# Kernel tuning notes

Measured on AMD Instinct MI355X. Metric: run time of the kernel, lower is better.

## Reference

```python
import jax, jax.numpy as jnp
import numpy as np

EPSILON = 1e-8
NUM_STEPS = 1000
S_OFFSET = 0.0001
POWER = 2
CLIPMAX = 0.999
B = 1048576


def _schedule():
    t = jnp.arange(0, NUM_STEPS + 1, dtype=jnp.float32)
    f_t = jnp.cos(np.pi / 2 * (t / NUM_STEPS + S_OFFSET) / (1 + S_OFFSET)) ** POWER
    alpha_bars = f_t / f_t[0]
    betas = jnp.concatenate([jnp.zeros([1], jnp.float32), 1.0 - alpha_bars[1:] / alpha_bars[:-1]])
    betas = jnp.minimum(betas, CLIPMAX)
    sigmas = jnp.sqrt(betas[1:] * ((1.0 - alpha_bars[:-1]) / (1.0 - alpha_bars[1:])))
    sigmas = jnp.concatenate([jnp.zeros([1], jnp.float32), sigmas])
    return alpha_bars, betas, sigmas


def setup_inputs() -> dict:
    key = jax.random.key(0)
    k1, k2, k3, k4, k5 = jax.random.split(key, 5)
    lt = jax.random.normal(k1, (B, 6), dtype=jnp.float32)
    predicted_l0 = jax.random.normal(k2, (B, 6), dtype=jnp.float32)
    pred_lattice = jax.random.normal(k3, (B, 3, 3), dtype=jnp.float32)
    z_noise = jax.random.normal(k4, (B, 6), dtype=jnp.float32)  # torch.randn_like(lt), frozen
    t = jax.random.randint(k5, (B,), 0, NUM_STEPS, dtype=jnp.int64)
    alpha_bars, betas, sigmas = _schedule()
    return {
        "lt": lt,
        "predicted_l0": predicted_l0,
        "pred_lattice": pred_lattice,
        "alpha_bars": alpha_bars,
        "betas": betas,
        "sigmas": sigmas,
        "z_noise": z_noise,
        "t": t,
    }


def reference(lt, predicted_l0, pred_lattice, alpha_bars, betas, sigmas, z_noise, t):
    # VP_lattice.reverse
    alpha = 1.0 - betas[t]
    alpha = jnp.maximum(alpha, 1.0 - betas[-2])  # clamp_min
    alpha_bar = alpha_bars[t]
    sigma = sigmas[t][:, None]

    # polar_decomposition: only the symmetric factor L_tilda = V diag(S) V^T is used
    _, S, Vt = jnp.linalg.svd(pred_lattice, full_matrices=False)  # (B,3),(B,3,3)
    L = jnp.einsum("bji,bj,bjk->bik", Vt, S, Vt)  # Vt^T @ diag(S) @ Vt
    L = (L + jnp.swapaxes(L, 1, 2)) / 2  # symmetrize

    # symmetric_matrix_to_vector: upper triangular incl. diagonal
    vec = jnp.stack([L[:, 0, 0], L[:, 0, 1], L[:, 0, 2], L[:, 1, 1], L[:, 1, 2], L[:, 2, 2]], axis=1)

    predicted_noise = lt - (vec + predicted_l0) / 2
    z = jnp.where((t > 1)[:, None], z_noise, jnp.zeros_like(z_noise))
    coef = (1.0 / jnp.sqrt(alpha + EPSILON))[:, None]
    scale = ((1.0 - alpha) / jnp.sqrt(1.0 - alpha_bar + EPSILON))[:, None]
    return coef * (lt - scale * predicted_noise) + sigma * z
```

## Files before the change

### kernel.cpp

```cpp
#include <hip/hip_runtime.h>


#define NUM_STEPS 1000
#define TBL 1008
#define BLOCK 256

__global__ __launch_bounds__(256) void sched_kernel(
    const float* __restrict__ alpha_bars,
    const float* __restrict__ betas,
    const float* __restrict__ sigmas,
    float* __restrict__ ws)
{
    int j = blockIdx.x * blockDim.x + threadIdx.x;
    if (j >= TBL) return;
    if (j <= NUM_STEPS) {
        float beta_last = betas[NUM_STEPS - 1];
        float alpha = 1.0f - fminf(betas[j], beta_last);
        float coef  = 1.0f / sqrtf(alpha + 1e-8f);
        float scale = (1.0f - alpha) / sqrtf(1.0f - alpha_bars[j] + 1e-8f);
        ws[j]           = coef * (1.0f - scale);
        ws[TBL + j]     = 0.5f * coef * scale;
        ws[2 * TBL + j] = (j > 1) ? sigmas[j] : 0.0f;
    } else {
        ws[j] = 0.0f; ws[TBL + j] = 0.0f; ws[2 * TBL + j] = 0.0f;
    }
}

__global__ __launch_bounds__(BLOCK, 6) void vp_lattice_kernel(
    const float* __restrict__ lt,
    const float* __restrict__ pl0,
    const float* __restrict__ plat,
    const float* __restrict__ alpha_bars,
    const float* __restrict__ betas,
    const float* __restrict__ sigmas,
    const float* __restrict__ z_noise,
    const int*   __restrict__ t,
    float* __restrict__ out,
    int n,
    const float* __restrict__ ws,
    int use_ws)
{
    __shared__ __align__(16) float sA[TBL];
    __shared__ __align__(16) float sB[TBL];
    __shared__ __align__(16) float sS[TBL];
    __shared__ __align__(16) float platT[BLOCK * 9];

    const int tid = threadIdx.x;
    const int rowBase = blockIdx.x * BLOCK;
    int rem = n - rowBase; if (rem > BLOCK) rem = BLOCK;

    if (rem == BLOCK) {
        const float4* g9 = reinterpret_cast<const float4*>(plat + (size_t)rowBase * 9);
        float4*       s9 = reinterpret_cast<float4*>(platT);
#pragma unroll
        for (int k = 0; k < 3; ++k) {
            int j = tid + k * BLOCK;
            if (j < BLOCK * 9 / 4) s9[j] = g9[j];
        }
    } else {
        for (int j = tid; j < rem * 9; j += BLOCK)
            platT[j] = plat[(size_t)rowBase * 9 + j];
    }

    if (use_ws) {
        const float4* w4 = reinterpret_cast<const float4*>(ws);
        float4* a4 = reinterpret_cast<float4*>(sA);
        float4* b4 = reinterpret_cast<float4*>(sB);
        float4* s4 = reinterpret_cast<float4*>(sS);
        for (int j = tid; j < TBL / 4; j += BLOCK) {
            a4[j] = w4[j];
            b4[j] = w4[TBL / 4 + j];
            s4[j] = w4[2 * (TBL / 4) + j];
        }
    } else {
        float beta_last = betas[NUM_STEPS - 1];
        for (int j = tid; j < TBL; j += BLOCK) {
            float A = 0.0f, Bc = 0.0f, S = 0.0f;
            if (j <= NUM_STEPS) {
                float alpha = 1.0f - fminf(betas[j], beta_last);
                float coef  = 1.0f / sqrtf(alpha + 1e-8f);
                float scale = (1.0f - alpha) / sqrtf(1.0f - alpha_bars[j] + 1e-8f);
                A  = coef * (1.0f - scale);
                Bc = 0.5f * coef * scale;
                S  = (j > 1) ? sigmas[j] : 0.0f;
            }
            sA[j] = A; sB[j] = Bc; sS[j] = S;
        }
    }

    int ti = (tid < rem) ? t[rowBase + tid] : 0;

    __syncthreads();

    if (tid >= rem) return;

    size_t b6 = (size_t)(rowBase + tid) * 6;
    const float2* lt2 = reinterpret_cast<const float2*>(lt + b6);
    const float2* p02 = reinterpret_cast<const float2*>(pl0 + b6);
    const float2* zn2 = reinterpret_cast<const float2*>(z_noise + b6);
    float2 lw0 = lt2[0], lw1 = lt2[1], lw2 = lt2[2];
    float2 pw0 = p02[0], pw1 = p02[1], pw2 = p02[2];
    float2 zw0 = zn2[0], zw1 = zn2[1], zw2 = zn2[2];

    const float* pr = platT + tid * 9;
    float a00 = pr[0], a01 = pr[1], a02 = pr[2];
    float a10 = pr[3], a11 = pr[4], a12 = pr[5];
    float a20 = pr[6], a21 = pr[7], a22 = pr[8];

    float m00 = a00*a00 + a10*a10 + a20*a20;
    float m01 = a00*a01 + a10*a11 + a20*a21;
    float m02 = a00*a02 + a10*a12 + a20*a22;
    float m11 = a01*a01 + a11*a11 + a21*a21;
    float m12 = a01*a02 + a11*a12 + a21*a22;
    float m22 = a02*a02 + a12*a12 + a22*a22;

    float q  = (m00 + m11 + m22) * (1.0f/3.0f);
    float b00 = m00 - q, b11 = m11 - q, b22 = m22 - q;
    float p1 = m01*m01 + m02*m02 + m12*m12;
    float p2 = b00*b00 + b11*b11 + b22*b22 + 2.0f*p1;
    float p  = sqrtf(p2 * (1.0f/6.0f));
    float detB = b00*(b11*b22 - m12*m12)
               - m01*(m01*b22 - m12*m02)
               + m02*(m01*m12 - b11*m02);
    float pinv = __fdividef(1.0f, fmaxf(p, 1e-20f));
    float r = 0.5f * detB * pinv * pinv * pinv;
    r = fminf(fmaxf(r, -1.0f), 1.0f);

    float ar = fabsf(r);
    float sq = sqrtf(1.0f - ar);
    float pl = 1.5707288f + ar * (-0.2121144f + ar * (0.0742610f - ar * 0.0187293f));
    float ac = sq * pl;
    float acr = (r >= 0.0f) ? ac : (3.14159265358979f - ac);
    float phi = acr * (1.0f/3.0f);
    float mu1 = q + 2.0f*p*__cosf(phi);
    float mu3 = q + 2.0f*p*__cosf(phi + 2.0943951023931953f);
    float mu2 = 3.0f*q - mu1 - mu3;
    float l1 = sqrtf(fmaxf(mu1, 0.0f));
    float l2 = sqrtf(fmaxf(mu2, 0.0f));
    float l3 = sqrtf(fmaxf(mu3, 0.0f));

    float IU   = l1 + l2 + l3;
    float IIU  = l1*(l2 + l3) + l2*l3;
    float IIIU = l1*l2*l3;
    float denom = (l1 + l2) * (l1 + l3) * (l2 + l3);
    float dinv  = __fdividef(1.0f, fmaxf(denom, 1e-25f));
    float sd = (IU*IU - IIU) * dinv;
    float td = IU * IIIU * dinv;
    float nd = -dinv;

    float mm00 = m00*m00 + m01*m01 + m02*m02;
    float mm01 = m00*m01 + m01*m11 + m02*m12;
    float mm02 = m00*m02 + m01*m12 + m02*m22;
    float mm11 = m01*m01 + m11*m11 + m12*m12;
    float mm12 = m01*m02 + m11*m12 + m12*m22;
    float mm22 = m02*m02 + m12*m12 + m22*m22;

    float v0 = nd*mm00 + sd*m00 + td;
    float v1 = nd*mm01 + sd*m01;
    float v2 = nd*mm02 + sd*m02;
    float v3 = nd*mm11 + sd*m11 + td;
    float v4 = nd*mm12 + sd*m12;
    float v5 = nd*mm22 + sd*m22 + td;

    float A  = sA[ti];
    float Bc = sB[ti];
    float S  = sS[ti];

    float2 o0, o1, o2;
    o0.x = A*lw0.x + Bc*(v0 + pw0.x) + S*zw0.x;
    o0.y = A*lw0.y + Bc*(v1 + pw0.y) + S*zw0.y;
    o1.x = A*lw1.x + Bc*(v2 + pw1.x) + S*zw1.x;
    o1.y = A*lw1.y + Bc*(v3 + pw1.y) + S*zw1.y;
    o2.x = A*lw2.x + Bc*(v4 + pw2.x) + S*zw2.x;
    o2.y = A*lw2.y + Bc*(v5 + pw2.y) + S*zw2.y;

    float2* out2 = reinterpret_cast<float2*>(out + b6);
    out2[0] = o0;
    out2[1] = o1;
    out2[2] = o2;
}

extern "C" void kernel_launch(void* const* d_in, const int* in_sizes, int n_in,
                              void* d_out, int out_size, void* d_ws, size_t ws_size,
                              hipStream_t stream) {
    const float* lt         = (const float*)d_in[0];
    const float* pl0        = (const float*)d_in[1];
    const float* plat       = (const float*)d_in[2];
    const float* alpha_bars = (const float*)d_in[3];
    const float* betas      = (const float*)d_in[4];
    const float* sigmas     = (const float*)d_in[5];
    const float* z_noise    = (const float*)d_in[6];
    const int*   t          = (const int*)d_in[7];
    float* out = (float*)d_out;
    float* ws  = (float*)d_ws;

    int n = in_sizes[0] / 6;
    int use_ws = (ws != nullptr && ws_size >= (size_t)(3 * TBL * sizeof(float)));

    if (use_ws) {
        sched_kernel<<<(TBL + 255) / 256, 256, 0, stream>>>(alpha_bars, betas, sigmas, ws);
    }
    int grid = (n + BLOCK - 1) / BLOCK;
    vp_lattice_kernel<<<grid, BLOCK, 0, stream>>>(
        lt, pl0, plat, alpha_bars, betas, sigmas, z_noise, t, out, n, ws, use_ws);
}
```

Before: 154.8 us.

## Process two rows per thread with float4 vectorized loads and stores

Result: no change. 155.0 us (+0.2%).

```diff
diff --git a/kernel.cpp b/kernel.cpp
--- a/kernel.cpp
+++ b/kernel.cpp
@@ -4,6 +4,8 @@
 #define NUM_STEPS 1000
 #define TBL 1008
 #define BLOCK 256
+#define ROWS 2
+#define RPB (BLOCK * ROWS)
 
 __global__ __launch_bounds__(256) void sched_kernel(
     const float* __restrict__ alpha_bars,
@@ -26,7 +28,70 @@
     }
 }
 
-__global__ __launch_bounds__(BLOCK, 6) void vp_lattice_kernel(
+__device__ __forceinline__ void sqrtm_vec(const float* __restrict__ pr,
+                                          float vv[6])
+{
+    float a00 = pr[0], a01 = pr[1], a02 = pr[2];
+    float a10 = pr[3], a11 = pr[4], a12 = pr[5];
+    float a20 = pr[6], a21 = pr[7], a22 = pr[8];
+
+    float m00 = a00*a00 + a10*a10 + a20*a20;
+    float m01 = a00*a01 + a10*a11 + a20*a21;
+    float m02 = a00*a02 + a10*a12 + a20*a22;
+    float m11 = a01*a01 + a11*a11 + a21*a21;
+    float m12 = a01*a02 + a11*a12 + a21*a22;
+    float m22 = a02*a02 + a12*a12 + a22*a22;
+
+    float q  = (m00 + m11 + m22) * (1.0f/3.0f);
+    float b00 = m00 - q, b11 = m11 - q, b22 = m22 - q;
+    float p1 = m01*m01 + m02*m02 + m12*m12;
+    float p2 = b00*b00 + b11*b11 + b22*b22 + 2.0f*p1;
+    float p  = sqrtf(p2 * (1.0f/6.0f));
+    float detB = b00*(b11*b22 - m12*m12)
+               - m01*(m01*b22 - m12*m02)
+               + m02*(m01*m12 - b11*m02);
+    float pinv = __fdividef(1.0f, fmaxf(p, 1e-20f));
+    float r = 0.5f * detB * pinv * pinv * pinv;
+    r = fminf(fmaxf(r, -1.0f), 1.0f);
+
+    float ar = fabsf(r);
+    float sq = sqrtf(1.0f - ar);
+    float pl = 1.5707288f + ar * (-0.2121144f + ar * (0.0742610f - ar * 0.0187293f));
+    float ac = sq * pl;
+    float acr = (r >= 0.0f) ? ac : (3.14159265358979f - ac);
+    float phi = acr * (1.0f/3.0f);
+    float mu1 = q + 2.0f*p*__cosf(phi);
+    float mu3 = q + 2.0f*p*__cosf(phi + 2.0943951023931953f);
+    float mu2 = 3.0f*q - mu1 - mu3;
+    float l1 = sqrtf(fmaxf(mu1, 0.0f));
+    float l2 = sqrtf(fmaxf(mu2, 0.0f));
+    float l3 = sqrtf(fmaxf(mu3, 0.0f));
+
+    float IU   = l1 + l2 + l3;
+    float IIU  = l1*(l2 + l3) + l2*l3;
+    float IIIU = l1*l2*l3;
+    float denom = (l1 + l2) * (l1 + l3) * (l2 + l3);
+    float dinv  = __fdividef(1.0f, fmaxf(denom, 1e-25f));
+    float sd = (IU*IU - IIU) * dinv;
+    float td = IU * IIIU * dinv;
+    float nd = -dinv;
+
+    float mm00 = m00*m00 + m01*m01 + m02*m02;
+    float mm01 = m00*m01 + m01*m11 + m02*m12;
+    float mm02 = m00*m02 + m01*m12 + m02*m22;
+    float mm11 = m01*m01 + m11*m11 + m12*m12;
+    float mm12 = m01*m02 + m11*m12 + m12*m22;
+    float mm22 = m02*m02 + m12*m12 + m22*m22;
+
+    vv[0] = nd*mm00 + sd*m00 + td;
+    vv[1] = nd*mm01 + sd*m01;
+    vv[2] = nd*mm02 + sd*m02;
+    vv[3] = nd*mm11 + sd*m11 + td;
+    vv[4] = nd*mm12 + sd*m12;
+    vv[5] = nd*mm22 + sd*m22 + td;
+}
+
+__global__ __launch_bounds__(BLOCK, 5) void vp_lattice_kernel(
     const float* __restrict__ lt,
     const float* __restrict__ pl0,
     const float* __restrict__ plat,
@@ -43,19 +108,20 @@
     __shared__ __align__(16) float sA[TBL];
     __shared__ __align__(16) float sB[TBL];
     __shared__ __align__(16) float sS[TBL];
-    __shared__ __align__(16) float platT[BLOCK * 9];
+    __shared__ __align__(16) float platT[RPB * 9];
 
     const int tid = threadIdx.x;
-    const int rowBase = blockIdx.x * BLOCK;
-    int rem = n - rowBase; if (rem > BLOCK) rem = BLOCK;
-
-    if (rem == BLOCK) {
+    const int rowBase = blockIdx.x * RPB;
+    int rem = n - rowBase; if (rem > RPB) rem = RPB;
+    const bool full = (rem == RPB);
+
+    if (full) {
         const float4* g9 = reinterpret_cast<const float4*>(plat + (size_t)rowBase * 9);
         float4*       s9 = reinterpret_cast<float4*>(platT);
 #pragma unroll
-        for (int k = 0; k < 3; ++k) {
+        for (int k = 0; k < 5; ++k) {
             int j = tid + k * BLOCK;
-            if (j < BLOCK * 9 / 4) s9[j] = g9[j];
+            if (j < RPB * 9 / 4) s9[j] = g9[j];
         }
     } else {
         for (int j = tid; j < rem * 9; j += BLOCK)
@@ -88,96 +154,79 @@
         }
     }
 
-    int ti = (tid < rem) ? t[rowBase + tid] : 0;
+    const int r0 = rowBase + 2 * tid;
+    int ti0 = 0, ti1 = 0;
+    float4 lv0, lv1, lv2, pv0, pv1, pv2, zv0, zv1, zv2;
+    lv0 = lv1 = lv2 = pv0 = pv1 = pv2 = zv0 = zv1 = zv2 = make_float4(0.f,0.f,0.f,0.f);
+
+    if (full) {
+        int2 tp = *(reinterpret_cast<const int2*>(t + rowBase) + tid);
+        ti0 = tp.x; ti1 = tp.y;
+        const float4* lp = reinterpret_cast<const float4*>(lt      + (size_t)rowBase * 6) + tid * 3;
+        const float4* pp = reinterpret_cast<const float4*>(pl0     + (size_t)rowBase * 6) + tid * 3;
+        const float4* zp = reinterpret_cast<const float4*>(z_noise + (size_t)rowBase * 6) + tid * 3;
+        lv0 = lp[0]; lv1 = lp[1]; lv2 = lp[2];
+        pv0 = pp[0]; pv1 = pp[1]; pv2 = pp[2];
+        zv0 = zp[0]; zv1 = zp[1]; zv2 = zp[2];
+    } else {
+        float lbuf[12] = {0}, pbuf[12] = {0}, zbuf[12] = {0};
+        for (int c = 0; c < 12; ++c) {
+            size_t idx = (size_t)r0 * 6 + c;
+            if (r0 * 6 + c < rem * 6 + rowBase * 6 && (r0 + c / 6) < n) {
+                lbuf[c] = lt[idx]; pbuf[c] = pl0[idx]; zbuf[c] = z_noise[idx];
+            }
+        }
+        lv0 = make_float4(lbuf[0], lbuf[1], lbuf[2], lbuf[3]);
+        lv1 = make_float4(lbuf[4], lbuf[5], lbuf[6], lbuf[7]);
+        lv2 = make_float4(lbuf[8], lbuf[9], lbuf[10], lbuf[11]);
+        pv0 = make_float4(pbuf[0], pbuf[1], pbuf[2], pbuf[3]);
+        pv1 = make_float4(pbuf[4], pbuf[5], pbuf[6], pbuf[7]);
+        pv2 = make_float4(pbuf[8], pbuf[9], pbuf[10], pbuf[11]);
+        zv0 = make_float4(zbuf[0], zbuf[1], zbuf[2], zbuf[3]);
+        zv1 = make_float4(zbuf[4], zbuf[5], zbuf[6], zbuf[7]);
+        zv2 = make_float4(zbuf[8], zbuf[9], zbuf[10], zbuf[11]);
+        if (r0     < n) ti0 = t[r0];
+        if (r0 + 1 < n) ti1 = t[r0 + 1];
+    }
 
     __syncthreads();
 
-    if (tid >= rem) return;
-
-    size_t b6 = (size_t)(rowBase + tid) * 6;
-    const float2* lt2 = reinterpret_cast<const float2*>(lt + b6);
-    const float2* p02 = reinterpret_cast<const float2*>(pl0 + b6);
-    const float2* zn2 = reinterpret_cast<const float2*>(z_noise + b6);
-    float2 lw0 = lt2[0], lw1 = lt2[1], lw2 = lt2[2];
-    float2 pw0 = p02[0], pw1 = p02[1], pw2 = p02[2];
-    float2 zw0 = zn2[0], zw1 = zn2[1], zw2 = zn2[2];
-
-    const float* pr = platT + tid * 9;
-    float a00 = pr[0], a01 = pr[1], a02 = pr[2];
-    float a10 = pr[3], a11 = pr[4], a12 = pr[5];
-    float a20 = pr[6], a21 = pr[7], a22 = pr[8];
-
-    float m00 = a00*a00 + a10*a10 + a20*a20;
-    float m01 = a00*a01 + a10*a11 + a20*a21;
-    float m02 = a00*a02 + a10*a12 + a20*a22;
-    float m11 = a01*a01 + a11*a11 + a21*a21;
-    float m12 = a01*a02 + a11*a12 + a21*a22;
-    float m22 = a02*a02 + a12*a12 + a22*a22;
-
-    float q  = (m00 + m11 + m22) * (1.0f/3.0f);
-    float b00 = m00 - q, b11 = m11 - q, b22 = m22 - q;
-    float p1 = m01*m01 + m02*m02 + m12*m12;
-    float p2 = b00*b00 + b11*b11 + b22*b22 + 2.0f*p1;
-    float p  = sqrtf(p2 * (1.0f/6.0f));
-    float detB = b00*(b11*b22 - m12*m12)
-               - m01*(m01*b22 - m12*m02)
-               + m02*(m01*m12 - b11*m02);
-    float pinv = __fdividef(1.0f, fmaxf(p, 1e-20f));
-    float r = 0.5f * detB * pinv * pinv * pinv;
-    r = fminf(fmaxf(r, -1.0f), 1.0f);
-
-    float ar = fabsf(r);
-    float sq = sqrtf(1.0f - ar);
-    float pl = 1.5707288f + ar * (-0.2121144f + ar * (0.0742610f - ar * 0.0187293f));
-    float ac = sq * pl;
-    float acr = (r >= 0.0f) ? ac : (3.14159265358979f - ac);
-    float phi = acr * (1.0f/3.0f);
-    float mu1 = q + 2.0f*p*__cosf(phi);
-    float mu3 = q + 2.0f*p*__cosf(phi + 2.0943951023931953f);
-    float mu2 = 3.0f*q - mu1 - mu3;
-    float l1 = sqrtf(fmaxf(mu1, 0.0f));
-    float l2 = sqrtf(fmaxf(mu2, 0.0f));
-    float l3 = sqrtf(fmaxf(mu3, 0.0f));
-
-    float IU   = l1 + l2 + l3;
-    float IIU  = l1*(l2 + l3) + l2*l3;
-    float IIIU = l1*l2*l3;
-    float denom = (l1 + l2) * (l1 + l3) * (l2 + l3);
-    float dinv  = __fdividef(1.0f, fmaxf(denom, 1e-25f));
-    float sd = (IU*IU - IIU) * dinv;
-    float td = IU * IIIU * dinv;
-    float nd = -dinv;
-
-    float mm00 = m00*m00 + m01*m01 + m02*m02;
-    float mm01 = m00*m01 + m01*m11 + m02*m12;
-    float mm02 = m00*m02 + m01*m12 + m02*m22;
-    float mm11 = m01*m01 + m11*m11 + m12*m12;
-    float mm12 = m01*m02 + m11*m12 + m12*m22;
-    float mm22 = m02*m02 + m12*m12 + m22*m22;
-
-    float v0 = nd*mm00 + sd*m00 + td;
-    float v1 = nd*mm01 + sd*m01;
-    float v2 = nd*mm02 + sd*m02;
-    float v3 = nd*mm11 + sd*m11 + td;
-    float v4 = nd*mm12 + sd*m12;
-    float v5 = nd*mm22 + sd*m22 + td;
-
-    float A  = sA[ti];
-    float Bc = sB[ti];
-    float S  = sS[ti];
-
-    float2 o0, o1, o2;
-    o0.x = A*lw0.x + Bc*(v0 + pw0.x) + S*zw0.x;
-    o0.y = A*lw0.y + Bc*(v1 + pw0.y) + S*zw0.y;
-    o1.x = A*lw1.x + Bc*(v2 + pw1.x) + S*zw1.x;
-    o1.y = A*lw1.y + Bc*(v3 + pw1.y) + S*zw1.y;
-    o2.x = A*lw2.x + Bc*(v4 + pw2.x) + S*zw2.x;
-    o2.y = A*lw2.y + Bc*(v5 + pw2.y) + S*zw2.y;
-
-    float2* out2 = reinterpret_cast<float2*>(out + b6);
-    out2[0] = o0;
-    out2[1] = o1;
-    out2[2] = o2;
+    if (r0 >= n) return;
+
+    float va[6];
+    sqrtm_vec(platT + tid * 18, va);
+    float A0 = sA[ti0], B0 = sB[ti0], S0 = sS[ti0];
+
+    float o[12];
+    o[0] = A0*lv0.x + B0*(va[0] + pv0.x) + S0*zv0.x;
+    o[1] = A0*lv0.y + B0*(va[1] + pv0.y) + S0*zv0.y;
+    o[2] = A0*lv0.z + B0*(va[2] + pv0.z) + S0*zv0.z;
+    o[3] = A0*lv0.w + B0*(va[3] + pv0.w) + S0*zv0.w;
+    o[4] = A0*lv1.x + B0*(va[4] + pv1.x) + S0*zv1.x;
+    o[5] = A0*lv1.y + B0*(va[5] + pv1.y) + S0*zv1.y;
+
+    bool has1 = (r0 + 1 < n);
+    if (has1) {
+        float vb[6];
+        sqrtm_vec(platT + tid * 18 + 9, vb);
+        float A1 = sA[ti1], B1 = sB[ti1], S1 = sS[ti1];
+        o[6]  = A1*lv1.z + B1*(vb[0] + pv1.z) + S1*zv1.z;
+        o[7]  = A1*lv1.w + B1*(vb[1] + pv1.w) + S1*zv1.w;
+        o[8]  = A1*lv2.x + B1*(vb[2] + pv2.x) + S1*zv2.x;
+        o[9]  = A1*lv2.y + B1*(vb[3] + pv2.y) + S1*zv2.y;
+        o[10] = A1*lv2.z + B1*(vb[4] + pv2.z) + S1*zv2.z;
+        o[11] = A1*lv2.w + B1*(vb[5] + pv2.w) + S1*zv2.w;
+    }
+
+    if (full) {
+        float4* op = reinterpret_cast<float4*>(out + (size_t)rowBase * 6) + tid * 3;
+        op[0] = make_float4(o[0], o[1], o[2],  o[3]);
+        op[1] = make_float4(o[4], o[5], o[6],  o[7]);
+        op[2] = make_float4(o[8], o[9], o[10], o[11]);
+    } else {
+        int lim = has1 ? 12 : 6;
+        for (int c = 0; c < lim; ++c) out[(size_t)r0 * 6 + c] = o[c];
+    }
 }
 
 extern "C" void kernel_launch(void* const* d_in, const int* in_sizes, int n_in,
@@ -200,7 +249,7 @@
     if (use_ws) {
         sched_kernel<<<(TBL + 255) / 256, 256, 0, stream>>>(alpha_bars, betas, sigmas, ws);
     }
-    int grid = (n + BLOCK - 1) / BLOCK;
+    int grid = (n + RPB - 1) / RPB;
     vp_lattice_kernel<<<grid, BLOCK, 0, stream>>>(
         lt, pl0, plat, alpha_bars, betas, sigmas, z_noise, t, out, n, ws, use_ws);
 }
```
